# Optimization experiments

Hardware: AMD Instinct MI355X
Metric: run time of the kernel (lower is better)

Reference implementation:

```python
import jax, jax.numpy as jnp
import numpy as np

N_SPECIES = 4  # species ids 0..3


def setup_inputs() -> dict:
    key = jax.random.key(0)
    k1, k2, k3, k4 = jax.random.split(key, 4)
    NTA, O, NMAX = 65536, 512, 512
    rho = jax.random.normal(k1, (NTA, O), dtype=jnp.float32)
    # per-species expert Linear(O -> NMAX): weights stacked [S, O, NMAX], bias [S, NMAX]
    W = jax.random.normal(k2, (N_SPECIES, O, NMAX), dtype=jnp.float32) * (1.0 / np.sqrt(O))
    b = jax.random.normal(k3, (N_SPECIES, NMAX), dtype=jnp.float32) * 0.01
    symbols = jax.random.randint(k4, (NTA,), 0, N_SPECIES, dtype=jnp.int32)
    return {"rho": rho, "W": W, "b": b, "symbols": symbols}


def reference(rho, W, b, symbols):
    # Faithful to Gj.forward: coeff[mask] = expert_spe(rho[mask]) for each species.
    # Vectorized form: apply each species' Linear to all atoms (dense GEMM),
    # then select per-atom by species mask. Loop is over the small fixed
    # species set (4), not over data dims.
    NTA = rho.shape[0]
    nmax = W.shape[-1]
    coeff = jnp.zeros((NTA, nmax), dtype=rho.dtype)
    for spe in range(W.shape[0]):
        y = rho @ W[spe] + b[spe]            # [NTA, nmax]
        mask = (symbols == spe)[:, None]      # [NTA, 1]
        coeff = jnp.where(mask, y, coeff)
    return coeff
```

## Files before the change

### kernel.cpp

```cpp
#include <hip/hip_runtime.h>


#define NTA   65536
#define DIM_O 512
#define NMAXD 512
#define NSPE  4

typedef __attribute__((ext_vector_type(4))) float  f32x4;
typedef __attribute__((ext_vector_type(8))) short  bf16x8;
typedef __attribute__((ext_vector_type(4))) short  bf16x4;

__device__ __forceinline__ short f2bf(float f) {
    unsigned u = __builtin_bit_cast(unsigned, f);
    u += 0x7FFFu + ((u >> 16) & 1u);
    return (short)(u >> 16);
}

__device__ __forceinline__ void bar_lds() {
    asm volatile("s_waitcnt lgkmcnt(0)" ::: "memory");
    __builtin_amdgcn_s_barrier();
    __builtin_amdgcn_sched_barrier(0);
}

__global__ void build_lists_kernel(const int* __restrict__ sym,
                                   int* __restrict__ counts,
                                   int* __restrict__ lists) {
    int i = blockIdx.x * 256 + threadIdx.x;
    int s = sym[i];
    int lane = threadIdx.x & 63;
    #pragma unroll
    for (int spe = 0; spe < NSPE; ++spe) {
        unsigned long long m = __ballot(s == spe);
        if (m == 0ull) continue;
        int leader = __ffsll(m) - 1;
        int base = 0;
        if (lane == leader) base = atomicAdd(&counts[spe], __popcll(m));
        base = __shfl(base, leader);
        if (s == spe) {
            int pos = __popcll(m & ((1ull << lane) - 1ull));
            lists[spe * NTA + base + pos] = i;
        }
    }
}

__global__ void pack_w_kernel(const float* __restrict__ W, short* __restrict__ Wp,
                              int* __restrict__ counts) {
    if (blockIdx.x == 0 && threadIdx.x < NSPE) counts[threadIdx.x] = 0;
    int idx = blockIdx.x * 256 + threadIdx.x;
    int j  = idx & 7;
    int l  = (idx >> 3) & 63;
    int nb = (idx >> 9) & 31;
    int kb = (idx >> 14) & 15;
    int s  = idx >> 18;
    int k = kb * 32 + (l >> 4) * 8 + j;
    int n = nb * 16 + (l & 15);
    Wp[idx] = f2bf(W[((size_t)s * DIM_O + k) * NMAXD + n]);
}

__global__ __launch_bounds__(768, 3)
void gemm_kernel(const float* __restrict__ rho,
                 const short* __restrict__ Wp,
                 const float* __restrict__ bias,
                 const int*  __restrict__ counts,
                 const int*  __restrict__ lists,
                 float* __restrict__ out)
{
    const int b    = blockIdx.x;
    const int tid  = threadIdx.x;
    const int lane = tid & 63;
    const int w    = tid >> 6;

    const int c0x = counts[0], c1x = counts[1], c2x = counts[2], c3x = counts[3];
    const int P1 = (c0x + 63) >> 6;
    const int P2 = P1 + ((c1x + 63) >> 6);
    const int P3 = P2 + ((c2x + 63) >> 6);
    const int ntot = P3 + ((c3x + 63) >> 6);
    if (b >= ntot) return;

    __shared__ int aidx[2][64];
    __shared__ __align__(16) short Abuf[2][64 * 64 * 8];

    #define TILE_INFO(ti, s_, mb_, cnt_)                                   \
        {   s_ = ((ti) >= P1) + ((ti) >= P2) + ((ti) >= P3);               \
            mb_ = (ti) - (s_ == 0 ? 0 : s_ == 1 ? P1 : s_ == 2 ? P2 : P3); \
            cnt_ = (s_ == 0 ? c0x : s_ == 1 ? c1x : s_ == 2 ? c2x : c3x); }

    const int pt    = tid - 512;
    const int scol8 = pt & 7;
    const int cc0   = scol8 >> 1;
    const int dof   = (scol8 & 1) * 4;

    #define GATHER(ti_, dstp_)                                              \
        {   int s2, mb2, cnt2; TILE_INFO(ti_, s2, mb2, cnt2);               \
            if (w == 8)                                                     \
                aidx[dstp_][lane] =                                         \
                    lists[s2 * NTA + min(mb2 * 64 + lane, cnt2 - 1)];       \
            _Pragma("unroll")                                               \
            for (int ps = 0; ps < 2; ++ps) {                                \
                const int srow = (pt >> 3) + ps * 32;                       \
                const int gi = lists[s2 * NTA + min(mb2 * 64 + srow, cnt2 - 1)]; \
                const float* g = rho + (size_t)gi * DIM_O + scol8 * 4;      \
                f32x4 v[16];                                                \
                _Pragma("unroll")                                           \
                for (int r = 0; r < 16; ++r) v[r] = *(const f32x4*)(g + r * 32); \
                const int roww = srow ^ ((cc0 & 3) << 1);                   \
                short* dstb = Abuf[dstp_];                                  \
                _Pragma("unroll")                                           \
                for (int r = 0; r < 16; ++r) {                              \
                    bf16x4 a;                                               \
                    _Pragma("unroll")                                       \
                    for (int q = 0; q < 4; ++q) a[q] = f2bf(v[r][q]);       \
                    *(bf16x4*)&dstb[((r * 4 + cc0) * 64 + roww) * 8 + dof] = a; \
                }                                                           \
            }                                                               \
        }

    if (w >= 8) GATHER(b, 0);
    bar_lds();

    int p = 0;
    for (int ti = b; ti < ntot; ti += 256, p ^= 1) {
        if (w < 8) {
            int s, mb, cnt; TILE_INFO(ti, s, mb, cnt);
            const int rows_here = min(64, cnt - mb * 64);
            const int lrow = lane & 15;
            const int lgr  = lane >> 4;
            const short* Ab = Abuf[p];
            const short* wbase = Wp + ((size_t)s * 512 + w * 4) * 512 + lane * 8;

            f32x4 acc[4][4];
            #pragma unroll
            for (int m = 0; m < 4; ++m)
                #pragma unroll
                for (int n = 0; n < 4; ++n) acc[m][n] = (f32x4)0.0f;

            #pragma unroll
            for (int kt = 0; kt < 8; ++kt) {
                bf16x8 bfr[2][4];
                #pragma unroll
                for (int ks = 0; ks < 2; ++ks)
                    #pragma unroll
                    for (int nf = 0; nf < 4; ++nf)
                        bfr[ks][nf] = *(const bf16x8*)
                            (wbase + (size_t)((kt * 2 + ks) * 32 + nf) * 512);
                #pragma unroll
                for (int ks = 0; ks < 2; ++ks) {
                    #pragma unroll
                    for (int mf = 0; mf < 4; ++mf) {
                        const int c = kt * 8 + ks * 4 + lgr;
                        const int r = (mf * 16 + lrow) ^ ((lgr & 3) << 1);
                        const bf16x8 afrag = *(const bf16x8*)&Ab[(c * 64 + r) * 8];
                        #pragma unroll
                        for (int nf = 0; nf < 4; ++nf)
                            acc[mf][nf] = __builtin_amdgcn_mfma_f32_16x16x32_bf16(
                                afrag, bfr[ks][nf], acc[mf][nf], 0, 0, 0);
                    }
                }
            }

            float bv[4];
            #pragma unroll
            for (int nf = 0; nf < 4; ++nf)
                bv[nf] = bias[s * NMAXD + w * 64 + nf * 16 + lrow];
            #pragma unroll
            for (int mf = 0; mf < 4; ++mf) {
                #pragma unroll
                for (int q = 0; q < 4; ++q) {
                    const int r = mf * 16 + lgr * 4 + q;
                    if (r < rows_here) {
                        float* orow = out + (size_t)aidx[p][r] * NMAXD + w * 64 + lrow;
                        #pragma unroll
                        for (int nf = 0; nf < 4; ++nf)
                            orow[nf * 16] = acc[mf][nf][q] + bv[nf];
                    }
                }
            }
        } else {
            const int tn = ti + 256;
            if (tn < ntot) GATHER(tn, p ^ 1);
        }
        bar_lds();
    }
    #undef GATHER
    #undef TILE_INFO
}

extern "C" void kernel_launch(void* const* d_in, const int* in_sizes, int n_in,
                              void* d_out, int out_size, void* d_ws, size_t ws_size,
                              hipStream_t stream) {
    const float* rho = (const float*)d_in[0];
    const float* W   = (const float*)d_in[1];
    const float* b   = (const float*)d_in[2];
    const int*   sym = (const int*)d_in[3];
    float* out = (float*)d_out;

    int*   counts = (int*)d_ws;
    int*   lists  = (int*)((char*)d_ws + 1024);
    short* Wp     = (short*)((char*)d_ws + 1024 + (size_t)NSPE * NTA * 4);

    pack_w_kernel<<<(NSPE * DIM_O * NMAXD) / 256, 256, 0, stream>>>(W, Wp, counts);
    build_lists_kernel<<<NTA / 256, 256, 0, stream>>>(sym, counts, lists);
    gemm_kernel<<<256, 768, 0, stream>>>(rho, Wp, b, counts, lists, out);
}
```

Baseline: 129.0 us.

## Double-buffer weight fragments in registers and widen gather warps to eight

Block size rises from 768 to 1024 threads, so eight producer wavefronts gather A rows instead of four, each handling one row instead of two. The compute wavefronts now prefetch the next k-step's B fragments, including the first fragments of the next tile, while the current MFMAs run, hiding global load latency. The cost is extra register pressure from the doubled B fragments, under launch bounds asking for 1024 threads with a minimum of 4 blocks, which could cause spills or lower occupancy.

```diff
diff --git a/kernel.cpp b/kernel.cpp
--- a/kernel.cpp
+++ b/kernel.cpp
@@ -57,7 +57,7 @@
     Wp[idx] = f2bf(W[((size_t)s * DIM_O + k) * NMAXD + n]);
 }
 
-__global__ __launch_bounds__(768, 3)
+__global__ __launch_bounds__(1024, 4)
 void gemm_kernel(const float* __restrict__ rho,
                  const short* __restrict__ Wp,
                  const float* __restrict__ bias,
@@ -86,8 +86,10 @@
             cnt_ = (s_ == 0 ? c0x : s_ == 1 ? c1x : s_ == 2 ? c2x : c3x); }
 
     const int pt    = tid - 512;
+    const int srow  = pt >> 3;
     const int scol8 = pt & 7;
     const int cc0   = scol8 >> 1;
+    const int roww  = srow ^ ((cc0 & 3) << 1);
     const int dof   = (scol8 & 1) * 4;
 
     #define GATHER(ti_, dstp_)                                              \
@@ -95,27 +97,40 @@
             if (w == 8)                                                     \
                 aidx[dstp_][lane] =                                         \
                     lists[s2 * NTA + min(mb2 * 64 + lane, cnt2 - 1)];       \
+            const int gi = lists[s2 * NTA + min(mb2 * 64 + srow, cnt2 - 1)];\
+            const float* g = rho + (size_t)gi * DIM_O + scol8 * 4;          \
+            f32x4 v[16];                                                    \
             _Pragma("unroll")                                               \
-            for (int ps = 0; ps < 2; ++ps) {                                \
-                const int srow = (pt >> 3) + ps * 32;                       \
-                const int gi = lists[s2 * NTA + min(mb2 * 64 + srow, cnt2 - 1)]; \
-                const float* g = rho + (size_t)gi * DIM_O + scol8 * 4;      \
-                f32x4 v[16];                                                \
+            for (int r = 0; r < 16; ++r) v[r] = *(const f32x4*)(g + r * 32);\
+            short* dstb = Abuf[dstp_];                                      \
+            _Pragma("unroll")                                               \
+            for (int r = 0; r < 16; ++r) {                                  \
+                bf16x4 a;                                                   \
                 _Pragma("unroll")                                           \
-                for (int r = 0; r < 16; ++r) v[r] = *(const f32x4*)(g + r * 32); \
-                const int roww = srow ^ ((cc0 & 3) << 1);                   \
-                short* dstb = Abuf[dstp_];                                  \
-                _Pragma("unroll")                                           \
-                for (int r = 0; r < 16; ++r) {                              \
-                    bf16x4 a;                                               \
-                    _Pragma("unroll")                                       \
-                    for (int q = 0; q < 4; ++q) a[q] = f2bf(v[r][q]);       \
-                    *(bf16x4*)&dstb[((r * 4 + cc0) * 64 + roww) * 8 + dof] = a; \
-                }                                                           \
+                for (int q = 0; q < 4; ++q) a[q] = f2bf(v[r][q]);           \
+                *(bf16x4*)&dstb[((r * 4 + cc0) * 64 + roww) * 8 + dof] = a; \
             }                                                               \
         }
 
-    if (w >= 8) GATHER(b, 0);
+    const int lrow = lane & 15;
+    const int lgr  = lane >> 4;
+
+    bf16x8 bfr[2][4];
+    #define LOAD_BFR(wb_, kt_)                                              \
+        _Pragma("unroll")                                                   \
+        for (int ks = 0; ks < 2; ++ks)                                      \
+            _Pragma("unroll")                                               \
+            for (int nf = 0; nf < 4; ++nf)                                  \
+                bfr[ks][nf] = *(const bf16x8*)                              \
+                    ((wb_) + (size_t)(((kt_) * 2 + ks) * 32 + nf) * 512);
+
+    if (w >= 8) {
+        GATHER(b, 0);
+    } else {
+        int s0, mb0, cnt0; TILE_INFO(b, s0, mb0, cnt0);
+        const short* wb0 = Wp + ((size_t)s0 * 512 + w * 4) * 512 + lane * 8;
+        LOAD_BFR(wb0, 0);
+    }
     bar_lds();
 
     int p = 0;
@@ -123,10 +138,9 @@
         if (w < 8) {
             int s, mb, cnt; TILE_INFO(ti, s, mb, cnt);
             const int rows_here = min(64, cnt - mb * 64);
-            const int lrow = lane & 15;
-            const int lgr  = lane >> 4;
             const short* Ab = Abuf[p];
             const short* wbase = Wp + ((size_t)s * 512 + w * 4) * 512 + lane * 8;
+            const int tn = ti + 256;
 
             f32x4 acc[4][4];
             #pragma unroll
@@ -136,13 +150,18 @@
 
             #pragma unroll
             for (int kt = 0; kt < 8; ++kt) {
-                bf16x8 bfr[2][4];
+                bf16x8 cur[2][4];
                 #pragma unroll
                 for (int ks = 0; ks < 2; ++ks)
                     #pragma unroll
-                    for (int nf = 0; nf < 4; ++nf)
-                        bfr[ks][nf] = *(const bf16x8*)
-                            (wbase + (size_t)((kt * 2 + ks) * 32 + nf) * 512);
+                    for (int nf = 0; nf < 4; ++nf) cur[ks][nf] = bfr[ks][nf];
+                if (kt < 7) {
+                    LOAD_BFR(wbase, kt + 1);
+                } else if (tn < ntot) {
+                    int s2, mb2, cnt2; TILE_INFO(tn, s2, mb2, cnt2);
+                    const short* wb2 = Wp + ((size_t)s2 * 512 + w * 4) * 512 + lane * 8;
+                    LOAD_BFR(wb2, 0);
+                }
                 #pragma unroll
                 for (int ks = 0; ks < 2; ++ks) {
                     #pragma unroll
@@ -153,7 +172,7 @@
                         #pragma unroll
                         for (int nf = 0; nf < 4; ++nf)
                             acc[mf][nf] = __builtin_amdgcn_mfma_f32_16x16x32_bf16(
-                                afrag, bfr[ks][nf], acc[mf][nf], 0, 0, 0);
+                                afrag, cur[ks][nf], acc[mf][nf], 0, 0, 0);
                     }
                 }
             }
@@ -182,6 +201,7 @@
         bar_lds();
     }
     #undef GATHER
+    #undef LOAD_BFR
     #undef TILE_INFO
 }
 
@@ -200,5 +220,5 @@
 
     pack_w_kernel<<<(NSPE * DIM_O * NMAXD) / 256, 256, 0, stream>>>(W, Wp, counts);
     build_lists_kernel<<<NTA / 256, 256, 0, stream>>>(sym, counts, lists);
-    gemm_kernel<<<256, 768, 0, stream>>>(rho, Wp, b, counts, lists, out);
-}
+    gemm_kernel<<<256, 1024, 0, stream>>>(rho, Wp, b, counts, lists, out);
+}
```

Result: slower. 201.5 us (+56.2%).
